# Performance work log

Measured on AMD Instinct MI355X. Metric: run time of the kernel, lower is better.

## Reference

```python
import jax, jax.numpy as jnp
import numpy as np

B, T, N, D, E = 16, 12, 512, 128, 32  # batch, time, nodes, model_dim, node_emb_dim


def setup_inputs() -> dict:
    key = jax.random.key(0)
    ks = jax.random.split(key, 7)
    return {
        "value": jax.random.normal(ks[0], (B, T, N, D), dtype=jnp.float32),
        "emb": jax.random.normal(ks[1], (T, N, E), dtype=jnp.float32),
        "attn_mask": jax.random.randint(ks[2], (B, N, N), 0, 2, dtype=jnp.int32),
        "W_qk": jax.random.normal(ks[3], (E, D), dtype=jnp.float32) * (1.0 / np.sqrt(E)),
        "b_qk": jax.random.normal(ks[4], (D,), dtype=jnp.float32) * 0.02,
        "W_v": jax.random.normal(ks[5], (D, D), dtype=jnp.float32) * (1.0 / np.sqrt(D)),
        "b_v": jax.random.normal(ks[6], (D,), dtype=jnp.float32) * 0.02,
    }


def reference(value, emb, attn_mask, W_qk, b_qk, W_v, b_v):
    # qk projection shared between query and key: [T, N, D]
    qk = emb @ W_qk + b_qk
    # query: softmax over feature dim D
    q = jax.nn.softmax(qk, axis=-1)                      # [T, N, D]
    # key: transpose then softmax over node dim N
    k = jax.nn.softmax(jnp.swapaxes(qk, -1, -2), axis=-1)  # [T, D, N]
    # value projection (note: out_proj in __init__ is unused in forward)
    v = value @ W_v + b_v                                # [B, T, N, D]
    # batch-independent base attention score, then broadcast over batch
    score = jnp.einsum('tnd,tdm->tnm', q, k)             # [T, N, N]
    score = jnp.broadcast_to(score[None], (value.shape[0],) + score.shape)  # [B, T, N, N]
    # masked fill: mask [B, N, N] -> [B, 1, N, N]
    score = jnp.where(attn_mask[:, None] == 0, jnp.float32(-1e9), score)
    out = jnp.einsum('btnm,btmd->btnd', score, v)         # [B, T, N, D]
    return out
```

## Files before the change

kernel.cpp:

```cpp
#include <hip/hip_runtime.h>

#define B_ 16
#define T_ 12
#define N_ 512
#define D_ 128
#define E_ 32

typedef __attribute__((ext_vector_type(8))) unsigned short u16x8;
typedef __attribute__((ext_vector_type(8))) __bf16 bf16x8;
typedef __attribute__((ext_vector_type(4))) float f32x4;

static __device__ __forceinline__ unsigned short f2bf(float f) {
    unsigned u = __float_as_uint(f);
    unsigned r = (u + 0x7fffu + ((u >> 16) & 1u)) >> 16;
    return (unsigned short)r;
}

__global__ __launch_bounds__(128) void kA1W(const float* __restrict__ emb,
                                            const float* __restrict__ Wqk,
                                            const float* __restrict__ bqk,
                                            float* __restrict__ qk,
                                            unsigned short* __restrict__ qb,
                                            const float* __restrict__ Wv,
                                            unsigned short* __restrict__ WvT) {
    if (blockIdx.x >= 6144) {
        int i = (blockIdx.x - 6144) * 128 + threadIdx.x;
        int d = i >> 7, k = i & 127;
        WvT[d * 128 + k] = f2bf(Wv[k * 128 + d]);
        return;
    }
    int tn = blockIdx.x;
    int d  = threadIdx.x;
    __shared__ float es[E_];
    if (d < E_) es[d] = emb[tn * E_ + d];
    __syncthreads();
    float acc = bqk[d];
#pragma unroll
    for (int e = 0; e < E_; ++e) acc = fmaf(es[e], Wqk[e * D_ + d], acc);
    qk[(size_t)tn * D_ + d] = acc;

    __shared__ float red[D_];
    red[d] = acc;
    __syncthreads();
#pragma unroll
    for (int s = 64; s > 0; s >>= 1) {
        if (d < s) red[d] = fmaxf(red[d], red[d + s]);
        __syncthreads();
    }
    float mx = red[0];
    __syncthreads();
    float ex = __expf(acc - mx);
    red[d] = ex;
    __syncthreads();
#pragma unroll
    for (int s = 64; s > 0; s >>= 1) {
        if (d < s) red[d] += red[d + s];
        __syncthreads();
    }
    qb[(size_t)tn * D_ + d] = f2bf(ex / red[0]);
}

__global__ __launch_bounds__(256) void kA2n(const float* __restrict__ qk,
                                            unsigned short* __restrict__ kN) {
    int t = blockIdx.x >> 4;
    int d0 = (blockIdx.x & 15) * 8;
    int tid = threadIdx.x;
    int dc = tid & 7, ni = tid >> 3;
    const float* base = qk + (size_t)t * N_ * D_ + d0 + dc;
    float vals[16];
    float mx = -1e30f;
#pragma unroll
    for (int j = 0; j < 16; ++j) {
        vals[j] = base[(size_t)(ni + 32 * j) * D_];
        mx = fmaxf(mx, vals[j]);
    }
    __shared__ float red[32][9];
    red[ni][dc] = mx;
    __syncthreads();
    if (tid < 8) {
        float m = red[0][tid];
#pragma unroll
        for (int r = 1; r < 32; ++r) m = fmaxf(m, red[r][tid]);
        red[0][tid] = m;
    }
    __syncthreads();
    mx = red[0][dc];
    float sum = 0.f;
#pragma unroll
    for (int j = 0; j < 16; ++j) {
        vals[j] = __expf(vals[j] - mx);
        sum += vals[j];
    }
    __syncthreads();
    red[ni][dc] = sum;
    __syncthreads();
    if (tid < 8) {
        float s = red[0][tid];
#pragma unroll
        for (int r = 1; r < 32; ++r) s += red[r][tid];
        red[0][tid] = s;
    }
    __syncthreads();
    float inv = 1.f / red[0][dc];
    unsigned short* op = kN + (size_t)t * N_ * D_ + d0 + dc;
#pragma unroll
    for (int j = 0; j < 16; ++j)
        op[(size_t)(ni + 32 * j) * D_] = f2bf(vals[j] * inv);
}

__global__ __launch_bounds__(256) void kF(const unsigned short* __restrict__ qb,
                                          const unsigned short* __restrict__ kN,
                                          unsigned short* __restrict__ sc,
                                          const float* __restrict__ value,
                                          const unsigned short* __restrict__ WvT,
                                          const float* __restrict__ bv,
                                          unsigned short* __restrict__ vT,
                                          const int* __restrict__ mask,
                                          unsigned* __restrict__ mb) {
    __shared__ unsigned short shl[2][128 * 72];
    int bid = blockIdx.x;
    int tid = threadIdx.x;

    if (bid >= 960) {
        int o = (bid - 960) * 256 + tid;
        const int* mp = mask + (size_t)o * 32;
        unsigned bits = 0;
#pragma unroll
        for (int j = 0; j < 32; j += 4) {
            int4 m4 = *(const int4*)&mp[j];
            bits |= (m4.x ? 1u : 0u) << j;
            bits |= (m4.y ? 1u : 0u) << (j + 1);
            bits |= (m4.z ? 1u : 0u) << (j + 2);
            bits |= (m4.w ? 1u : 0u) << (j + 3);
        }
        mb[o] = bits;
        return;
    }

    int wave = tid >> 6, lane = tid & 63;
    int q = lane >> 4, lr = lane & 15;
    int rbase = (wave & 1) * 64, cbase = (wave >> 1) * 64;

    f32x4 acc[4][4];
#pragma unroll
    for (int i = 0; i < 4; ++i)
#pragma unroll
        for (int j = 0; j < 4; ++j) acc[i][j] = (f32x4){0.f, 0.f, 0.f, 0.f};

    if (bid < 192) {
        int mt = bid & 3, nt = (bid >> 2) & 3, t = bid >> 4;
        int n0 = nt * 128, m0 = mt * 128;
        unsigned short* Qs = shl[0];
        unsigned short* Ks = shl[1];
        const unsigned short* qp = qb + (size_t)t * N_ * D_ + (size_t)n0 * D_;
        const unsigned short* kp = kN + (size_t)t * N_ * D_ + (size_t)m0 * D_;

        for (int c = 0; c < 2; ++c) {
            int k0 = c * 64;
            __syncthreads();
#pragma unroll
            for (int i = 0; i < 4; ++i) {
                int lin = tid + i * 256;
                int r = lin >> 3, seg = lin & 7;
                *(u16x8*)&Qs[r * 72 + seg * 8] =
                    *(const u16x8*)&qp[(size_t)r * D_ + k0 + seg * 8];
                *(u16x8*)&Ks[r * 72 + seg * 8] =
                    *(const u16x8*)&kp[(size_t)r * D_ + k0 + seg * 8];
            }
            __syncthreads();
#pragma unroll
            for (int kk = 0; kk < 2; ++kk) {
                bf16x8 a[4], b[4];
#pragma unroll
                for (int i = 0; i < 4; ++i)
                    a[i] = *(const bf16x8*)&Qs[(rbase + 16 * i + lr) * 72 + kk * 32 + q * 8];
#pragma unroll
                for (int j = 0; j < 4; ++j)
                    b[j] = *(const bf16x8*)&Ks[(cbase + 16 * j + lr) * 72 + kk * 32 + q * 8];
#pragma unroll
                for (int i = 0; i < 4; ++i)
#pragma unroll
                    for (int j = 0; j < 4; ++j)
                        acc[i][j] = __builtin_amdgcn_mfma_f32_16x16x32_bf16(
                            a[i], b[j], acc[i][j], 0, 0, 0);
            }
        }
        unsigned short* sp = sc + (size_t)t * N_ * N_;
#pragma unroll
        for (int i = 0; i < 4; ++i)
#pragma unroll
            for (int j = 0; j < 4; ++j) {
                int row0 = n0 + rbase + 16 * i + q * 4;
                int col = m0 + cbase + 16 * j + lr;
#pragma unroll
                for (int e = 0; e < 4; ++e)
                    sp[(size_t)(row0 + e) * N_ + col] = f2bf(acc[i][j][e]);
            }
        return;
    }

    {
        int idx = bid - 192;
        int mt = idx & 3, bt = idx >> 2;
        int m0 = mt * 128;
        unsigned short* Ws = shl[0];
        unsigned short* Vs = shl[1];
        const float* vp = value + ((size_t)bt * N_ + m0) * D_;

        for (int c = 0; c < 2; ++c) {
            int k0 = c * 64;
            __syncthreads();
#pragma unroll
            for (int i = 0; i < 4; ++i) {
                int lin = tid + i * 256;
                int r = lin >> 3, seg = lin & 7;
                *(u16x8*)&Ws[r * 72 + seg * 8] =
                    *(const u16x8*)&WvT[r * 128 + k0 + seg * 8];
            }
#pragma unroll
            for (int i = 0; i < 8; ++i) {
                int lin = tid + i * 256;
                int r = lin >> 4, c4 = lin & 15;
                float4 f = *(const float4*)&vp[(size_t)r * D_ + k0 + c4 * 4];
                ushort4 o;
                o.x = f2bf(f.x); o.y = f2bf(f.y); o.z = f2bf(f.z); o.w = f2bf(f.w);
                *(ushort4*)&Vs[r * 72 + c4 * 4] = o;
            }
            __syncthreads();
#pragma unroll
            for (int kk = 0; kk < 2; ++kk) {
                bf16x8 a[4], b[4];
#pragma unroll
                for (int i = 0; i < 4; ++i)
                    a[i] = *(const bf16x8*)&Ws[(rbase + 16 * i + lr) * 72 + kk * 32 + q * 8];
#pragma unroll
                for (int j = 0; j < 4; ++j)
                    b[j] = *(const bf16x8*)&Vs[(cbase + 16 * j + lr) * 72 + kk * 32 + q * 8];
#pragma unroll
                for (int i = 0; i < 4; ++i)
#pragma unroll
                    for (int j = 0; j < 4; ++j)
                        acc[i][j] = __builtin_amdgcn_mfma_f32_16x16x32_bf16(
                            a[i], b[j], acc[i][j], 0, 0, 0);
            }
        }
        unsigned short* op = vT + (size_t)bt * N_ * D_;
#pragma unroll
        for (int i = 0; i < 4; ++i) {
            int row0 = rbase + 16 * i + q * 4;
#pragma unroll
            for (int j = 0; j < 4; ++j) {
                int col = m0 + cbase + 16 * j + lr;
#pragma unroll
                for (int e = 0; e < 4; ++e)
                    op[(size_t)(row0 + e) * N_ + col] = f2bf(acc[i][j][e] + bv[row0 + e]);
            }
        }
    }
}

__global__ __launch_bounds__(256) void kC(const unsigned short* __restrict__ sc,
                                          const unsigned* __restrict__ mb,
                                          const unsigned short* __restrict__ vT,
                                          float* __restrict__ out) {
    int n0 = blockIdx.x * 128;
    int t = blockIdx.y, b = blockIdx.z;
    int tid = threadIdx.x;
    int wave = tid >> 6, lane = tid & 63;
    int q = lane >> 4, lr = lane & 15;
    int rbase = (wave & 1) * 64, cbase = (wave >> 1) * 64;

    __shared__ unsigned short Ss[128 * 72];
    __shared__ unsigned short Vs[128 * 72];

    const unsigned short* scp = sc + (size_t)t * N_ * N_ + (size_t)n0 * N_;
    const unsigned short* vtp = vT + ((size_t)(b * T_ + t)) * N_ * D_;
    const unsigned* mbp = mb + ((size_t)b * N_ + n0) * 16;

    const unsigned short NEG = 0xCE6E;

    f32x4 acc[4][4];
#pragma unroll
    for (int i = 0; i < 4; ++i)
#pragma unroll
        for (int j = 0; j < 4; ++j) acc[i][j] = (f32x4){0.f, 0.f, 0.f, 0.f};

    int sr = tid >> 1, sh2 = tid & 1;
    const unsigned short* sg = scp + (size_t)sr * N_ + sh2 * 32;
    const unsigned short* vg = vtp + (size_t)sr * N_ + sh2 * 32;
    const unsigned* mwp = mbp + sr * 16 + sh2;

    u16x8 sreg[4], vreg[4];
    unsigned mw;
#pragma unroll
    for (int p = 0; p < 4; ++p) {
        sreg[p] = *(const u16x8*)(sg + p * 8);
        vreg[p] = *(const u16x8*)(vg + p * 8);
    }
    mw = mwp[0];

    for (int kc = 0; kc < 8; ++kc) {
        if (kc) __syncthreads();
        unsigned short* Sd = &Ss[sr * 72 + sh2 * 32];
        unsigned short* Vd = &Vs[sr * 72 + sh2 * 32];
#pragma unroll
        for (int p = 0; p < 4; ++p) {
            unsigned bits = mw >> (p * 8);
            u16x8 o;
#pragma unroll
            for (int j = 0; j < 8; ++j)
                o[j] = ((bits >> j) & 1u) ? sreg[p][j] : NEG;
            *(u16x8*)(Sd + p * 8) = o;
            *(u16x8*)(Vd + p * 8) = vreg[p];
        }
        __syncthreads();
        if (kc < 7) {
            int off = (kc + 1) * 64;
#pragma unroll
            for (int p = 0; p < 4; ++p) {
                sreg[p] = *(const u16x8*)(sg + off + p * 8);
                vreg[p] = *(const u16x8*)(vg + off + p * 8);
            }
            mw = mwp[(kc + 1) * 2];
        }
#pragma unroll
        for (int ks = 0; ks < 2; ++ks) {
            bf16x8 a[4], bfr[4];
#pragma unroll
            for (int i = 0; i < 4; ++i)
                a[i] = *(const bf16x8*)&Ss[(rbase + 16 * i + lr) * 72 + ks * 32 + q * 8];
#pragma unroll
            for (int j = 0; j < 4; ++j)
                bfr[j] = *(const bf16x8*)&Vs[(cbase + 16 * j + lr) * 72 + ks * 32 + q * 8];
#pragma unroll
            for (int i = 0; i < 4; ++i)
#pragma unroll
                for (int j = 0; j < 4; ++j)
                    acc[i][j] = __builtin_amdgcn_mfma_f32_16x16x32_bf16(
                        a[i], bfr[j], acc[i][j], 0, 0, 0);
        }
    }

    float* ob = out + ((size_t)(b * T_ + t)) * N_ * D_;
#pragma unroll
    for (int i = 0; i < 4; ++i) {
#pragma unroll
        for (int j = 0; j < 4; ++j) {
            int row0 = n0 + rbase + 16 * i + q * 4;
            int col = cbase + 16 * j + lr;
#pragma unroll
            for (int e = 0; e < 4; ++e)
                ob[(size_t)(row0 + e) * D_ + col] = acc[i][j][e];
        }
    }
}

extern "C" void kernel_launch(void* const* d_in, const int* in_sizes, int n_in,
                              void* d_out, int out_size, void* d_ws, size_t ws_size,
                              hipStream_t stream) {
    const float* value = (const float*)d_in[0];
    const float* emb   = (const float*)d_in[1];
    const int*   mask  = (const int*)d_in[2];
    const float* Wqk   = (const float*)d_in[3];
    const float* bqk   = (const float*)d_in[4];
    const float* Wv    = (const float*)d_in[5];
    const float* bvv   = (const float*)d_in[6];
    float* out = (float*)d_out;

    float* ws = (float*)d_ws;
    float*          qkf  = ws;
    unsigned short* qb   = (unsigned short*)(ws + 786432);
    unsigned short* kNb  = (unsigned short*)(ws + 1179648);
    unsigned short* scb  = (unsigned short*)(ws + 1572864);
    unsigned short* vtb  = (unsigned short*)(ws + 3145728);
    unsigned short* WvTb = (unsigned short*)(ws + 9437184);
    unsigned*       mbp  = (unsigned*)(ws + 9445376);

    kA1W<<<6272, 128, 0, stream>>>(emb, Wqk, bqk, qkf, qb, Wv, WvTb);
    kA2n<<<192, 256, 0, stream>>>(qkf, kNb);
    kF<<<1472, 256, 0, stream>>>(qb, kNb, scb, value, WvTb, bvv, vtb, mask, mbp);
    kC<<<dim3(4, T_, B_), 256, 0, stream>>>(scb, mbp, vtb, out);
}
```

Measured before the change: 167.4 us.

## Load MFMA operands straight from global memory, drop LDS staging and syncs

All three GEMM paths (score, value projection, masked score@V) now read each wave's MFMA fragments directly from global memory into registers instead of staging tiles through LDS with barriers. The mask is applied per fragment from the packed bit words. The softmax reductions in the two small kernels move from LDS tree reductions to wavefront shuffles. This removes LDS traffic and barrier stalls and frees LDS for occupancy, at the cost of redundant, less coalesced global and L2 reads, since each fragment row is fetched by several waves. The register double-buffering prefetch in the main kernel is also gone.

```diff
diff --git a/kernel.cpp b/kernel.cpp
--- a/kernel.cpp
+++ b/kernel.cpp
@@ -14,6 +14,10 @@
     unsigned u = __float_as_uint(f);
     unsigned r = (u + 0x7fffu + ((u >> 16) & 1u)) >> 16;
     return (unsigned short)r;
+}
+
+static __device__ __forceinline__ bf16x8 bc(u16x8 u) {
+    return __builtin_bit_cast(bf16x8, u);
 }
 
 __global__ __launch_bounds__(128) void kA1W(const float* __restrict__ emb,
@@ -39,25 +43,22 @@
     for (int e = 0; e < E_; ++e) acc = fmaf(es[e], Wqk[e * D_ + d], acc);
     qk[(size_t)tn * D_ + d] = acc;
 
-    __shared__ float red[D_];
-    red[d] = acc;
-    __syncthreads();
-#pragma unroll
-    for (int s = 64; s > 0; s >>= 1) {
-        if (d < s) red[d] = fmaxf(red[d], red[d + s]);
-        __syncthreads();
-    }
-    float mx = red[0];
-    __syncthreads();
+    int wv = d >> 6, lane = d & 63;
+    float mx = acc;
+#pragma unroll
+    for (int s = 32; s > 0; s >>= 1) mx = fmaxf(mx, __shfl_xor(mx, s));
+    __shared__ float wred[2][2];
+    if (lane == 0) wred[0][wv] = mx;
+    __syncthreads();
+    mx = fmaxf(wred[0][0], wred[0][1]);
     float ex = __expf(acc - mx);
-    red[d] = ex;
-    __syncthreads();
-#pragma unroll
-    for (int s = 64; s > 0; s >>= 1) {
-        if (d < s) red[d] += red[d + s];
-        __syncthreads();
-    }
-    qb[(size_t)tn * D_ + d] = f2bf(ex / red[0]);
+    float sum = ex;
+#pragma unroll
+    for (int s = 32; s > 0; s >>= 1) sum += __shfl_xor(sum, s);
+    if (lane == 0) wred[1][wv] = sum;
+    __syncthreads();
+    sum = wred[1][0] + wred[1][1];
+    qb[(size_t)tn * D_ + d] = f2bf(ex / sum);
 }
 
 __global__ __launch_bounds__(256) void kA2n(const float* __restrict__ qk,
@@ -74,34 +75,26 @@
         vals[j] = base[(size_t)(ni + 32 * j) * D_];
         mx = fmaxf(mx, vals[j]);
     }
-    __shared__ float red[32][9];
-    red[ni][dc] = mx;
-    __syncthreads();
-    if (tid < 8) {
-        float m = red[0][tid];
-#pragma unroll
-        for (int r = 1; r < 32; ++r) m = fmaxf(m, red[r][tid]);
-        red[0][tid] = m;
-    }
-    __syncthreads();
-    mx = red[0][dc];
+#pragma unroll
+    for (int s = 8; s < 64; s <<= 1) mx = fmaxf(mx, __shfl_xor(mx, s));
+    __shared__ float red[2][4][8];
+    int wv = tid >> 6;
+    if ((tid & 63) < 8) red[0][wv][dc] = mx;
+    __syncthreads();
+    mx = fmaxf(fmaxf(red[0][0][dc], red[0][1][dc]),
+               fmaxf(red[0][2][dc], red[0][3][dc]));
     float sum = 0.f;
 #pragma unroll
     for (int j = 0; j < 16; ++j) {
         vals[j] = __expf(vals[j] - mx);
         sum += vals[j];
     }
-    __syncthreads();
-    red[ni][dc] = sum;
-    __syncthreads();
-    if (tid < 8) {
-        float s = red[0][tid];
-#pragma unroll
-        for (int r = 1; r < 32; ++r) s += red[r][tid];
-        red[0][tid] = s;
-    }
-    __syncthreads();
-    float inv = 1.f / red[0][dc];
+#pragma unroll
+    for (int s = 8; s < 64; s <<= 1) sum += __shfl_xor(sum, s);
+    if ((tid & 63) < 8) red[1][wv][dc] = sum;
+    __syncthreads();
+    sum = red[1][0][dc] + red[1][1][dc] + red[1][2][dc] + red[1][3][dc];
+    float inv = 1.f / sum;
     unsigned short* op = kN + (size_t)t * N_ * D_ + d0 + dc;
 #pragma unroll
     for (int j = 0; j < 16; ++j)
@@ -117,7 +110,6 @@
                                           unsigned short* __restrict__ vT,
                                           const int* __restrict__ mask,
                                           unsigned* __restrict__ mb) {
-    __shared__ unsigned short shl[2][128 * 72];
     int bid = blockIdx.x;
     int tid = threadIdx.x;
 
@@ -150,40 +142,27 @@
     if (bid < 192) {
         int mt = bid & 3, nt = (bid >> 2) & 3, t = bid >> 4;
         int n0 = nt * 128, m0 = mt * 128;
-        unsigned short* Qs = shl[0];
-        unsigned short* Ks = shl[1];
         const unsigned short* qp = qb + (size_t)t * N_ * D_ + (size_t)n0 * D_;
         const unsigned short* kp = kN + (size_t)t * N_ * D_ + (size_t)m0 * D_;
-
-        for (int c = 0; c < 2; ++c) {
-            int k0 = c * 64;
-            __syncthreads();
-#pragma unroll
-            for (int i = 0; i < 4; ++i) {
-                int lin = tid + i * 256;
-                int r = lin >> 3, seg = lin & 7;
-                *(u16x8*)&Qs[r * 72 + seg * 8] =
-                    *(const u16x8*)&qp[(size_t)r * D_ + k0 + seg * 8];
-                *(u16x8*)&Ks[r * 72 + seg * 8] =
-                    *(const u16x8*)&kp[(size_t)r * D_ + k0 + seg * 8];
-            }
-            __syncthreads();
-#pragma unroll
-            for (int kk = 0; kk < 2; ++kk) {
-                bf16x8 a[4], b[4];
-#pragma unroll
-                for (int i = 0; i < 4; ++i)
-                    a[i] = *(const bf16x8*)&Qs[(rbase + 16 * i + lr) * 72 + kk * 32 + q * 8];
+        const unsigned short* ar[4];
+        const unsigned short* br[4];
+#pragma unroll
+        for (int i = 0; i < 4; ++i) ar[i] = qp + (size_t)(rbase + 16 * i + lr) * D_ + q * 8;
+#pragma unroll
+        for (int j = 0; j < 4; ++j) br[j] = kp + (size_t)(cbase + 16 * j + lr) * D_ + q * 8;
+#pragma unroll
+        for (int kk = 0; kk < 4; ++kk) {
+            bf16x8 a[4], b[4];
+#pragma unroll
+            for (int i = 0; i < 4; ++i) a[i] = bc(*(const u16x8*)(ar[i] + kk * 32));
+#pragma unroll
+            for (int j = 0; j < 4; ++j) b[j] = bc(*(const u16x8*)(br[j] + kk * 32));
+#pragma unroll
+            for (int i = 0; i < 4; ++i)
 #pragma unroll
                 for (int j = 0; j < 4; ++j)
-                    b[j] = *(const bf16x8*)&Ks[(cbase + 16 * j + lr) * 72 + kk * 32 + q * 8];
-#pragma unroll
-                for (int i = 0; i < 4; ++i)
-#pragma unroll
-                    for (int j = 0; j < 4; ++j)
-                        acc[i][j] = __builtin_amdgcn_mfma_f32_16x16x32_bf16(
-                            a[i], b[j], acc[i][j], 0, 0, 0);
-            }
+                    acc[i][j] = __builtin_amdgcn_mfma_f32_16x16x32_bf16(
+                        a[i], b[j], acc[i][j], 0, 0, 0);
         }
         unsigned short* sp = sc + (size_t)t * N_ * N_;
 #pragma unroll
@@ -203,46 +182,33 @@
         int idx = bid - 192;
         int mt = idx & 3, bt = idx >> 2;
         int m0 = mt * 128;
-        unsigned short* Ws = shl[0];
-        unsigned short* Vs = shl[1];
         const float* vp = value + ((size_t)bt * N_ + m0) * D_;
-
-        for (int c = 0; c < 2; ++c) {
-            int k0 = c * 64;
-            __syncthreads();
-#pragma unroll
-            for (int i = 0; i < 4; ++i) {
-                int lin = tid + i * 256;
-                int r = lin >> 3, seg = lin & 7;
-                *(u16x8*)&Ws[r * 72 + seg * 8] =
-                    *(const u16x8*)&WvT[r * 128 + k0 + seg * 8];
+        const unsigned short* wr_[4];
+        const float* vr_[4];
+#pragma unroll
+        for (int i = 0; i < 4; ++i) wr_[i] = WvT + (rbase + 16 * i + lr) * 128 + q * 8;
+#pragma unroll
+        for (int j = 0; j < 4; ++j) vr_[j] = vp + (size_t)(cbase + 16 * j + lr) * D_ + q * 8;
+#pragma unroll
+        for (int kk = 0; kk < 4; ++kk) {
+            bf16x8 a[4], b[4];
+#pragma unroll
+            for (int i = 0; i < 4; ++i) a[i] = bc(*(const u16x8*)(wr_[i] + kk * 32));
+#pragma unroll
+            for (int j = 0; j < 4; ++j) {
+                float4 f0 = *(const float4*)(vr_[j] + kk * 32);
+                float4 f1 = *(const float4*)(vr_[j] + kk * 32 + 4);
+                u16x8 o;
+                o[0] = f2bf(f0.x); o[1] = f2bf(f0.y); o[2] = f2bf(f0.z); o[3] = f2bf(f0.w);
+                o[4] = f2bf(f1.x); o[5] = f2bf(f1.y); o[6] = f2bf(f1.z); o[7] = f2bf(f1.w);
+                b[j] = bc(o);
             }
 #pragma unroll
-            for (int i = 0; i < 8; ++i) {
-                int lin = tid + i * 256;
-                int r = lin >> 4, c4 = lin & 15;
-                float4 f = *(const float4*)&vp[(size_t)r * D_ + k0 + c4 * 4];
-                ushort4 o;
-                o.x = f2bf(f.x); o.y = f2bf(f.y); o.z = f2bf(f.z); o.w = f2bf(f.w);
-                *(ushort4*)&Vs[r * 72 + c4 * 4] = o;
-            }
-            __syncthreads();
-#pragma unroll
-            for (int kk = 0; kk < 2; ++kk) {
-                bf16x8 a[4], b[4];
-#pragma unroll
-                for (int i = 0; i < 4; ++i)
-                    a[i] = *(const bf16x8*)&Ws[(rbase + 16 * i + lr) * 72 + kk * 32 + q * 8];
+            for (int i = 0; i < 4; ++i)
 #pragma unroll
                 for (int j = 0; j < 4; ++j)
-                    b[j] = *(const bf16x8*)&Vs[(cbase + 16 * j + lr) * 72 + kk * 32 + q * 8];
-#pragma unroll
-                for (int i = 0; i < 4; ++i)
-#pragma unroll
-                    for (int j = 0; j < 4; ++j)
-                        acc[i][j] = __builtin_amdgcn_mfma_f32_16x16x32_bf16(
-                            a[i], b[j], acc[i][j], 0, 0, 0);
-            }
+                    acc[i][j] = __builtin_amdgcn_mfma_f32_16x16x32_bf16(
+                        a[i], b[j], acc[i][j], 0, 0, 0);
         }
         unsigned short* op = vT + (size_t)bt * N_ * D_;
 #pragma unroll
@@ -270,9 +236,6 @@
     int q = lane >> 4, lr = lane & 15;
     int rbase = (wave & 1) * 64, cbase = (wave >> 1) * 64;
 
-    __shared__ unsigned short Ss[128 * 72];
-    __shared__ unsigned short Vs[128 * 72];
-
     const unsigned short* scp = sc + (size_t)t * N_ * N_ + (size_t)n0 * N_;
     const unsigned short* vtp = vT + ((size_t)(b * T_ + t)) * N_ * D_;
     const unsigned* mbp = mb + ((size_t)b * N_ + n0) * 16;
@@ -285,60 +248,38 @@
 #pragma unroll
         for (int j = 0; j < 4; ++j) acc[i][j] = (f32x4){0.f, 0.f, 0.f, 0.f};
 
-    int sr = tid >> 1, sh2 = tid & 1;
-    const unsigned short* sg = scp + (size_t)sr * N_ + sh2 * 32;
-    const unsigned short* vg = vtp + (size_t)sr * N_ + sh2 * 32;
-    const unsigned* mwp = mbp + sr * 16 + sh2;
-
-    u16x8 sreg[4], vreg[4];
-    unsigned mw;
-#pragma unroll
-    for (int p = 0; p < 4; ++p) {
-        sreg[p] = *(const u16x8*)(sg + p * 8);
-        vreg[p] = *(const u16x8*)(vg + p * 8);
-    }
-    mw = mwp[0];
-
-    for (int kc = 0; kc < 8; ++kc) {
-        if (kc) __syncthreads();
-        unsigned short* Sd = &Ss[sr * 72 + sh2 * 32];
-        unsigned short* Vd = &Vs[sr * 72 + sh2 * 32];
-#pragma unroll
-        for (int p = 0; p < 4; ++p) {
-            unsigned bits = mw >> (p * 8);
+    const unsigned short* ar[4];
+    const unsigned* mr[4];
+    const unsigned short* br[4];
+#pragma unroll
+    for (int i = 0; i < 4; ++i) {
+        int r = rbase + 16 * i + lr;
+        ar[i] = scp + (size_t)r * N_ + q * 8;
+        mr[i] = mbp + r * 16;
+    }
+#pragma unroll
+    for (int j = 0; j < 4; ++j) br[j] = vtp + (size_t)(cbase + 16 * j + lr) * N_ + q * 8;
+
+#pragma unroll 4
+    for (int kc = 0; kc < 16; ++kc) {
+        bf16x8 a[4], bb[4];
+#pragma unroll
+        for (int i = 0; i < 4; ++i) {
+            u16x8 s = *(const u16x8*)(ar[i] + kc * 32);
+            unsigned bits = mr[i][kc] >> (q * 8);
             u16x8 o;
 #pragma unroll
-            for (int j = 0; j < 8; ++j)
-                o[j] = ((bits >> j) & 1u) ? sreg[p][j] : NEG;
-            *(u16x8*)(Sd + p * 8) = o;
-            *(u16x8*)(Vd + p * 8) = vreg[p];
-        }
-        __syncthreads();
-        if (kc < 7) {
-            int off = (kc + 1) * 64;
-#pragma unroll
-            for (int p = 0; p < 4; ++p) {
-                sreg[p] = *(const u16x8*)(sg + off + p * 8);
-                vreg[p] = *(const u16x8*)(vg + off + p * 8);
-            }
-            mw = mwp[(kc + 1) * 2];
-        }
-#pragma unroll
-        for (int ks = 0; ks < 2; ++ks) {
-            bf16x8 a[4], bfr[4];
-#pragma unroll
-            for (int i = 0; i < 4; ++i)
-                a[i] = *(const bf16x8*)&Ss[(rbase + 16 * i + lr) * 72 + ks * 32 + q * 8];
+            for (int e = 0; e < 8; ++e) o[e] = ((bits >> e) & 1u) ? s[e] : NEG;
+            a[i] = bc(o);
+        }
+#pragma unroll
+        for (int j = 0; j < 4; ++j) bb[j] = bc(*(const u16x8*)(br[j] + kc * 32));
+#pragma unroll
+        for (int i = 0; i < 4; ++i)
 #pragma unroll
             for (int j = 0; j < 4; ++j)
-                bfr[j] = *(const bf16x8*)&Vs[(cbase + 16 * j + lr) * 72 + ks * 32 + q * 8];
-#pragma unroll
-            for (int i = 0; i < 4; ++i)
-#pragma unroll
-                for (int j = 0; j < 4; ++j)
-                    acc[i][j] = __builtin_amdgcn_mfma_f32_16x16x32_bf16(
-                        a[i], bfr[j], acc[i][j], 0, 0, 0);
-        }
+                acc[i][j] = __builtin_amdgcn_mfma_f32_16x16x32_bf16(
+                    a[i], bb[j], acc[i][j], 0, 0, 0);
     }
 
     float* ob = out + ((size_t)(b * T_ + t)) * N_ * D_;
```

After: 198.4 us. 18.5% more time.

## Double-buffer V tiles via direct global-to-LDS loads with XOR swizzle in kC

Applied to the files above, without the earlier changes.

The score-times-V kernel now streams the V tile straight into a double-buffered LDS region using global_load_lds, prefetching the next chunk while MFMAs run on the current one. LDS padding is replaced with an XOR swizzle for both the masked score tile and the V tile. The per-chunk barrier structure is reworked and launch bounds now request three blocks per CU. The two softmax kernels also switch from shared-memory tree reductions to wave shuffles, which removes several barriers. The risks are that completion of the async LDS loads relies on the compiler's vmcnt waits for the sreg loads, and the extra LDS buffer may limit occupancy.

```diff
diff --git a/kernel.cpp b/kernel.cpp
--- a/kernel.cpp
+++ b/kernel.cpp
@@ -39,25 +39,22 @@
     for (int e = 0; e < E_; ++e) acc = fmaf(es[e], Wqk[e * D_ + d], acc);
     qk[(size_t)tn * D_ + d] = acc;
 
-    __shared__ float red[D_];
-    red[d] = acc;
+    int wv = d >> 6, lane = d & 63;
+    float mx = acc;
+#pragma unroll
+    for (int s = 32; s > 0; s >>= 1) mx = fmaxf(mx, __shfl_xor(mx, s));
+    __shared__ float wred[2][2];
+    if (lane == 0) wred[0][wv] = mx;
     __syncthreads();
-#pragma unroll
-    for (int s = 64; s > 0; s >>= 1) {
-        if (d < s) red[d] = fmaxf(red[d], red[d + s]);
-        __syncthreads();
-    }
-    float mx = red[0];
+    mx = fmaxf(wred[0][0], wred[0][1]);
+    float ex = __expf(acc - mx);
+    float sum = ex;
+#pragma unroll
+    for (int s = 32; s > 0; s >>= 1) sum += __shfl_xor(sum, s);
+    if (lane == 0) wred[1][wv] = sum;
     __syncthreads();
-    float ex = __expf(acc - mx);
-    red[d] = ex;
-    __syncthreads();
-#pragma unroll
-    for (int s = 64; s > 0; s >>= 1) {
-        if (d < s) red[d] += red[d + s];
-        __syncthreads();
-    }
-    qb[(size_t)tn * D_ + d] = f2bf(ex / red[0]);
+    sum = wred[1][0] + wred[1][1];
+    qb[(size_t)tn * D_ + d] = f2bf(ex / sum);
 }
 
 __global__ __launch_bounds__(256) void kA2n(const float* __restrict__ qk,
@@ -74,34 +71,26 @@
         vals[j] = base[(size_t)(ni + 32 * j) * D_];
         mx = fmaxf(mx, vals[j]);
     }
-    __shared__ float red[32][9];
-    red[ni][dc] = mx;
+#pragma unroll
+    for (int s = 8; s < 64; s <<= 1) mx = fmaxf(mx, __shfl_xor(mx, s));
+    __shared__ float red[2][4][8];
+    int wv = tid >> 6;
+    if ((tid & 63) < 8) red[0][wv][dc] = mx;
     __syncthreads();
-    if (tid < 8) {
-        float m = red[0][tid];
-#pragma unroll
-        for (int r = 1; r < 32; ++r) m = fmaxf(m, red[r][tid]);
-        red[0][tid] = m;
-    }
-    __syncthreads();
-    mx = red[0][dc];
+    mx = fmaxf(fmaxf(red[0][0][dc], red[0][1][dc]),
+               fmaxf(red[0][2][dc], red[0][3][dc]));
     float sum = 0.f;
 #pragma unroll
     for (int j = 0; j < 16; ++j) {
         vals[j] = __expf(vals[j] - mx);
         sum += vals[j];
     }
+#pragma unroll
+    for (int s = 8; s < 64; s <<= 1) sum += __shfl_xor(sum, s);
+    if ((tid & 63) < 8) red[1][wv][dc] = sum;
     __syncthreads();
-    red[ni][dc] = sum;
-    __syncthreads();
-    if (tid < 8) {
-        float s = red[0][tid];
-#pragma unroll
-        for (int r = 1; r < 32; ++r) s += red[r][tid];
-        red[0][tid] = s;
-    }
-    __syncthreads();
-    float inv = 1.f / red[0][dc];
+    sum = red[1][0][dc] + red[1][1][dc] + red[1][2][dc] + red[1][3][dc];
+    float inv = 1.f / sum;
     unsigned short* op = kN + (size_t)t * N_ * D_ + d0 + dc;
 #pragma unroll
     for (int j = 0; j < 16; ++j)
@@ -259,10 +248,10 @@
     }
 }
 
-__global__ __launch_bounds__(256) void kC(const unsigned short* __restrict__ sc,
-                                          const unsigned* __restrict__ mb,
-                                          const unsigned short* __restrict__ vT,
-                                          float* __restrict__ out) {
+__global__ __launch_bounds__(256, 3) void kC(const unsigned short* __restrict__ sc,
+                                             const unsigned* __restrict__ mb,
+                                             const unsigned short* __restrict__ vT,
+                                             float* __restrict__ out) {
     int n0 = blockIdx.x * 128;
     int t = blockIdx.y, b = blockIdx.z;
     int tid = threadIdx.x;
@@ -270,13 +259,12 @@
     int q = lane >> 4, lr = lane & 15;
     int rbase = (wave & 1) * 64, cbase = (wave >> 1) * 64;
 
-    __shared__ unsigned short Ss[128 * 72];
-    __shared__ unsigned short Vs[128 * 72];
+    __shared__ unsigned short Sb[128 * 64];
+    __shared__ unsigned short Vb[2][128 * 64];
 
     const unsigned short* scp = sc + (size_t)t * N_ * N_ + (size_t)n0 * N_;
     const unsigned short* vtp = vT + ((size_t)(b * T_ + t)) * N_ * D_;
     const unsigned* mbp = mb + ((size_t)b * N_ + n0) * 16;
-
     const unsigned short NEG = 0xCE6E;
 
     f32x4 acc[4][4];
@@ -287,22 +275,34 @@
 
     int sr = tid >> 1, sh2 = tid & 1;
     const unsigned short* sg = scp + (size_t)sr * N_ + sh2 * 32;
-    const unsigned short* vg = vtp + (size_t)sr * N_ + sh2 * 32;
     const unsigned* mwp = mbp + sr * 16 + sh2;
-
-    u16x8 sreg[4], vreg[4];
+    int swz_r = (sr & 7) << 4;
+    char* Sw[4];
+#pragma unroll
+    for (int p = 0; p < 4; ++p)
+        Sw[p] = (char*)Sb + sr * 128 + ((sh2 * 64 + p * 16) ^ swz_r);
+
+    int l3 = lane >> 3, l7 = lane & 7;
+    int vin = (l7 * 16) ^ (l3 << 4);
+    const char* vbase = (const char*)vtp;
+
+#pragma unroll
+    for (int it = 0; it < 4; ++it) {
+        int row = (it * 4 + wave) * 8 + l3;
+        const char* src = vbase + (size_t)row * 1024 + vin;
+        char* dst = (char*)&Vb[0][0] + ((it * 4 + wave) * 64 + lane) * 16;
+        __builtin_amdgcn_global_load_lds(
+            (const __attribute__((address_space(1))) unsigned*)src,
+            (__attribute__((address_space(3))) unsigned*)dst, 16, 0, 0);
+    }
+    u16x8 sreg[4];
     unsigned mw;
 #pragma unroll
-    for (int p = 0; p < 4; ++p) {
-        sreg[p] = *(const u16x8*)(sg + p * 8);
-        vreg[p] = *(const u16x8*)(vg + p * 8);
-    }
+    for (int p = 0; p < 4; ++p) sreg[p] = *(const u16x8*)(sg + p * 8);
     mw = mwp[0];
 
     for (int kc = 0; kc < 8; ++kc) {
-        if (kc) __syncthreads();
-        unsigned short* Sd = &Ss[sr * 72 + sh2 * 32];
-        unsigned short* Vd = &Vs[sr * 72 + sh2 * 32];
+        int cur = kc & 1;
 #pragma unroll
         for (int p = 0; p < 4; ++p) {
             unsigned bits = mw >> (p * 8);
@@ -310,35 +310,54 @@
 #pragma unroll
             for (int j = 0; j < 8; ++j)
                 o[j] = ((bits >> j) & 1u) ? sreg[p][j] : NEG;
-            *(u16x8*)(Sd + p * 8) = o;
-            *(u16x8*)(Vd + p * 8) = vreg[p];
-        }
-        __syncthreads();
+            *(u16x8*)Sw[p] = o;
+        }
         if (kc < 7) {
-            int off = (kc + 1) * 64;
-#pragma unroll
-            for (int p = 0; p < 4; ++p) {
-                sreg[p] = *(const u16x8*)(sg + off + p * 8);
-                vreg[p] = *(const u16x8*)(vg + off + p * 8);
-            }
+            int off = (kc + 1) * 128;
+#pragma unroll
+            for (int it = 0; it < 4; ++it) {
+                int row = (it * 4 + wave) * 8 + l3;
+                const char* src = vbase + (size_t)row * 1024 + off + vin;
+                char* dst = (char*)&Vb[cur ^ 1][0] + ((it * 4 + wave) * 64 + lane) * 16;
+                __builtin_amdgcn_global_load_lds(
+                    (const __attribute__((address_space(1))) unsigned*)src,
+                    (__attribute__((address_space(3))) unsigned*)dst, 16, 0, 0);
+            }
+            int eoff = (kc + 1) * 64;
+#pragma unroll
+            for (int p = 0; p < 4; ++p) sreg[p] = *(const u16x8*)(sg + eoff + p * 8);
             mw = mwp[(kc + 1) * 2];
         }
-#pragma unroll
-        for (int ks = 0; ks < 2; ++ks) {
-            bf16x8 a[4], bfr[4];
-#pragma unroll
-            for (int i = 0; i < 4; ++i)
-                a[i] = *(const bf16x8*)&Ss[(rbase + 16 * i + lr) * 72 + ks * 32 + q * 8];
-#pragma unroll
-            for (int j = 0; j < 4; ++j)
-                bfr[j] = *(const bf16x8*)&Vs[(cbase + 16 * j + lr) * 72 + ks * 32 + q * 8];
-#pragma unroll
-            for (int i = 0; i < 4; ++i)
-#pragma unroll
-                for (int j = 0; j < 4; ++j)
-                    acc[i][j] = __builtin_amdgcn_mfma_f32_16x16x32_bf16(
-                        a[i], bfr[j], acc[i][j], 0, 0, 0);
-        }
+        asm volatile("s_waitcnt lgkmcnt(0)" ::: "memory");
+        __builtin_amdgcn_s_barrier();
+        __builtin_amdgcn_sched_barrier(0);
+        {
+            const char* Sbase = (const char*)Sb;
+            const char* Vbase = (const char*)&Vb[cur][0];
+            int swz_l = (lr & 7) << 4;
+#pragma unroll
+            for (int ks = 0; ks < 2; ++ks) {
+                bf16x8 a[4], bb[4];
+#pragma unroll
+                for (int i = 0; i < 4; ++i) {
+                    int r = rbase + 16 * i + lr;
+                    a[i] = *(const bf16x8*)(Sbase + r * 128 + ((ks * 64 + q * 16) ^ swz_l));
+                }
+#pragma unroll
+                for (int j = 0; j < 4; ++j) {
+                    int d = cbase + 16 * j + lr;
+                    bb[j] = *(const bf16x8*)(Vbase + d * 128 + ((ks * 64 + q * 16) ^ swz_l));
+                }
+#pragma unroll
+                for (int i = 0; i < 4; ++i)
+#pragma unroll
+                    for (int j = 0; j < 4; ++j)
+                        acc[i][j] = __builtin_amdgcn_mfma_f32_16x16x32_bf16(
+                            a[i], bb[j], acc[i][j], 0, 0, 0);
+            }
+        }
+        __builtin_amdgcn_s_barrier();
+        __builtin_amdgcn_sched_barrier(0);
     }
 
     float* ob = out + ((size_t)(b * T_ + t)) * N_ * D_;
```

Result: faster. 161.8 us (-3.4%).
